# Kernel tuning notes

Hardware: AMD Instinct MI355X
Metric: run time of the kernel (lower is better)

Reference implementation:

```python
import jax, jax.numpy as jnp
import numpy as np

B, C, H, W = 16, 128, 56, 56
QK, HEADS, NWIN, TOPK, MLPR = 128, 4, 7, 4, 3
HD_Q, HD_V = QK // HEADS, C // HEADS
WH, WW = H // NWIN, W // NWIN          # 8, 8 tokens per window side
P2, W2 = NWIN * NWIN, WH * WW          # 49 regions, 64 tokens/region
SCALE = QK ** -0.5                     # BiFormer uses full qk_dim**-0.5 for both router and pixel attn


def _dwconv(x, w, b):
    # x: (B,C,H,W); w: (C,1,k,k) depthwise, odd k with SAME padding == torch padding=k//2
    y = jax.lax.conv_general_dilated(x, w, (1, 1), 'SAME',
                                     feature_group_count=x.shape[1],
                                     dimension_numbers=('NCHW', 'OIHW', 'NCHW'))
    return y + b[None, :, None, None]


def _ln(x, g, b):
    m = x.mean(-1, keepdims=True)
    v = ((x - m) ** 2).mean(-1, keepdims=True)
    return (x - m) * jax.lax.rsqrt(v + 1e-6) * g + b


def _win(t):  # (B,H,W,c) -> (B,P2,WH,WW,c)
    b, _, _, c = t.shape
    return t.reshape(b, NWIN, WH, NWIN, WW, c).transpose(0, 1, 3, 2, 4, 5).reshape(b, P2, WH, WW, c)


def _unwin(t):  # (B,P2,W2,c) -> (B,H,W,c)
    b, c = t.shape[0], t.shape[-1]
    return t.reshape(b, NWIN, NWIN, WH, WW, c).transpose(0, 1, 3, 2, 4, 5).reshape(b, H, W, c)


def setup_inputs() -> dict:
    key = jax.random.key(0)
    ks = jax.random.split(key, 8)
    p = lambda k, sh: (0.02 * jax.random.normal(k, sh)).astype(jnp.float32)
    return {
        'x': jax.random.normal(ks[0], (B, C, H, W), dtype=jnp.float32),
        'pos_w': p(ks[1], (C, 1, 3, 3)), 'pos_b': jnp.zeros((C,), jnp.float32),
        'ln1_g': jnp.ones((C,), jnp.float32), 'ln1_b': jnp.zeros((C,), jnp.float32),
        'qkv_w': p(ks[2], (C, 2 * QK + C)), 'qkv_b': jnp.zeros((2 * QK + C,), jnp.float32),
        'lepe_w': p(ks[3], (C, 1, 5, 5)), 'lepe_b': jnp.zeros((C,), jnp.float32),
        'wo_w': p(ks[4], (C, C)), 'wo_b': jnp.zeros((C,), jnp.float32),
        'ln2_g': jnp.ones((C,), jnp.float32), 'ln2_b': jnp.zeros((C,), jnp.float32),
        'mlp_w1': p(ks[5], (C, MLPR * C)), 'mlp_b1': jnp.zeros((MLPR * C,), jnp.float32),
        'mlp_w2': p(ks[6], (MLPR * C, C)), 'mlp_b2': jnp.zeros((C,), jnp.float32),
    }


def reference(x, pos_w, pos_b, ln1_g, ln1_b, qkv_w, qkv_b, lepe_w, lepe_b,
              wo_w, wo_b, ln2_g, ln2_b, mlp_w1, mlp_b1, mlp_w2, mlp_b2):
    # CPE: x = x + depthwise3x3(x)
    x = x + _dwconv(x, pos_w, pos_b)
    xh = x.transpose(0, 2, 3, 1)                        # NHWC

    # ---- BiLevelRoutingAttention(norm1(x)) ----
    y = _ln(xh, ln1_g, ln1_b)
    qkv = y @ qkv_w + qkv_b                             # (B,H,W,2*QK+C)
    q, kv = qkv[..., :QK], qkv[..., QK:]                # kv = [k | v]
    qw, kvw = _win(q), _win(kv)                         # (B,P2,WH,WW,.)

    # region-level routing: detached window means, coarse affinity, top-k regions
    q_win = jax.lax.stop_gradient(qw.mean((2, 3)))      # (B,P2,QK)
    k_win = jax.lax.stop_gradient(kvw[..., :QK].mean((2, 3)))
    logits = jnp.einsum('bpc,bqc->bpq', q_win * SCALE, k_win)
    _, idx = jax.lax.top_k(logits, TOPK)                # (B,P2,TOPK) int32

    # gather k/v tokens of the selected regions (mul_weight='none': weights unused)
    kv_pix = kvw.reshape(B, P2, W2, QK + C)
    kv_sel = jax.vmap(lambda t, i: t[i])(kv_pix, idx)   # (B,P2,TOPK,W2,QK+C)
    k_sel = kv_sel[..., :QK].reshape(B, P2, TOPK * W2, HEADS, HD_Q)
    v_sel = kv_sel[..., QK:].reshape(B, P2, TOPK * W2, HEADS, HD_V)
    q_pix = qw.reshape(B, P2, W2, HEADS, HD_Q)

    att = jnp.einsum('bpqhd,bpkhd->bphqk', q_pix * SCALE, k_sel)
    att = jax.nn.softmax(att, axis=-1)
    o = jnp.einsum('bphqk,bpkhd->bpqhd', att, v_sel).reshape(B, P2, W2, C)
    o = _unwin(o)                                       # (B,H,W,C)

    # LePE: depthwise 5x5 on v over the full image, then output projection
    v_img = kv[..., QK:].transpose(0, 3, 1, 2)
    lepe = _dwconv(v_img, lepe_w, lepe_b).transpose(0, 2, 3, 1)
    o = (o + lepe) @ wo_w + wo_b
    xh = xh + o

    # ---- MLP(norm2(x)) ----
    z = _ln(xh, ln2_g, ln2_b)
    z = jax.nn.gelu(z @ mlp_w1 + mlp_b1, approximate=False) @ mlp_w2 + mlp_b2
    xh = xh + z
    return xh.transpose(0, 3, 1, 2)                     # back to NCHW
```

## Files before the change

kernel.cpp:

```cpp
#include <hip/hip_runtime.h>
#include <math.h>

#define BATCH 16
#define CH    128
#define HGT   56
#define WID   56
#define NPIX  (BATCH*HGT*WID)
#define NQKV  384
#define NWIN  7
#define P2    49
#define TOPK  4
#define ATT_SCALE 0.088388347648318447f

typedef __attribute__((ext_vector_type(8))) short short8;
typedef __attribute__((ext_vector_type(4))) short short4v;
typedef __attribute__((ext_vector_type(4))) float float4v;

static __device__ __forceinline__ unsigned short f2bf(float f) {
  unsigned u = __float_as_uint(f);
  u += 0x7fffu + ((u >> 16) & 1u);
  return (unsigned short)(u >> 16);
}
static __device__ __forceinline__ float bf2f(unsigned short u) {
  return __uint_as_float((unsigned)u << 16);
}

__global__ __launch_bounds__(128) void k_prep(
    const float* __restrict__ qkv_w, const float* __restrict__ wo_w,
    const float* __restrict__ mlp_w1, const float* __restrict__ mlp_w2,
    unsigned short* __restrict__ Wq, unsigned short* __restrict__ Wo,
    unsigned short* __restrict__ W1, unsigned short* __restrict__ W2) {
  int bx = blockIdx.x, t = threadIdx.x;
  if (bx < 384) {
    int n = bx;
    Wq[n*128 + t] = f2bf(qkv_w[(size_t)t*384 + n]);
  } else if (bx < 512) {
    int n = bx - 384;
    Wo[n*128 + t] = f2bf(wo_w[(size_t)t*128 + n]);
  } else if (bx < 896) {
    int n = bx - 512;
    W1[n*128 + t] = f2bf(mlp_w1[(size_t)t*384 + n]);
  } else {
    int n = bx - 896;
    for (int k = t; k < 384; k += 128)
      W2[n*384 + k] = f2bf(mlp_w2[(size_t)k*128 + n]);
  }
}

__global__ __launch_bounds__(256) void k_posconv(const float* __restrict__ x,
    const float* __restrict__ pw, const float* __restrict__ pb,
    float* __restrict__ xh) {
  __shared__ float sh[10*58*32];
  int b = blockIdx.y;
  int rg = blockIdx.x >> 2, cg = blockIdx.x & 3;
  int row0 = rg*8, c0 = cg*32;
  int t = threadIdx.x;
  for (int i = t; i < 10*58*32/4; i += 256)
    ((int4*)sh)[i] = make_int4(0,0,0,0);
  __syncthreads();
  for (int i = t; i < 4480; i += 256) {
    int c = i & 31, chunk = (i >> 5) % 14, rr = i / 448;
    int grow = row0 + rr - 1;
    if ((unsigned)grow < HGT) {
      float4 v = *(const float4*)(x + ((size_t)(b*CH + c0 + c))*(HGT*WID)
                                  + grow*WID + chunk*4);
      float* d = &sh[(rr*58 + 1 + chunk*4)*32 + c];
      d[0] = v.x; d[32] = v.y; d[64] = v.z; d[96] = v.w;
    }
  }
  __syncthreads();
  int c = t & 31, pg = t >> 5;
  float w[9];
#pragma unroll
  for (int i = 0; i < 9; i++) w[i] = pw[(c0 + c)*9 + i];
  float bias = pb[c0 + c];
  const float* rowp[3];
#pragma unroll
  for (int dy = 0; dy < 3; dy++) rowp[dy] = &sh[((pg + dy)*58)*32 + c];
  float win[3][3];
#pragma unroll
  for (int j = 0; j < 2; j++)
#pragma unroll
    for (int dy = 0; dy < 3; dy++) win[j][dy] = rowp[dy][j*32];
  float* ob = &xh[(((size_t)b*HGT + row0 + pg)*WID)*CH + c0 + c];
#pragma unroll
  for (int col = 0; col < 56; col++) {
    int slot = (col + 2) % 3;
#pragma unroll
    for (int dy = 0; dy < 3; dy++) win[slot][dy] = rowp[dy][(col + 2)*32];
    float s = bias + win[(col + 1) % 3][1];
#pragma unroll
    for (int dx = 0; dx < 3; dx++) {
      int sl = (col + dx) % 3;
#pragma unroll
      for (int dy = 0; dy < 3; dy++) s += win[sl][dy] * w[dy*3 + dx];
    }
    ob[col*CH] = s;
  }
}

__global__ __launch_bounds__(256) void k_route(const float* __restrict__ xh,
    const float* __restrict__ g, const float* __restrict__ be,
    const float* __restrict__ qkv_w, const float* __restrict__ qkv_b,
    float* __restrict__ qwin, float* __restrict__ kwin) {
  __shared__ float yt[128*68];
  __shared__ float ym[128];
  int bp = blockIdx.x; int b = bp / P2, p = bp % P2;
  int wy = p / NWIN, wx = p % NWIN;
  int t = threadIdx.x;
  int pl = t >> 2, qu = t & 3;
  {
    int hg = wy*8 + (pl >> 3), wg = wx*8 + (pl & 7);
    const float4* src = (const float4*)(xh + (((size_t)b*HGT + hg)*WID + wg)*CH + qu*32);
    float v[32]; float s = 0.f, ss = 0.f;
#pragma unroll
    for (int i = 0; i < 8; i++) {
      float4 f = src[i];
      v[4*i] = f.x; v[4*i+1] = f.y; v[4*i+2] = f.z; v[4*i+3] = f.w;
      s += f.x + f.y + f.z + f.w;
      ss += f.x*f.x + f.y*f.y + f.z*f.z + f.w*f.w;
    }
    s += __shfl_xor(s, 1); ss += __shfl_xor(ss, 1);
    s += __shfl_xor(s, 2); ss += __shfl_xor(ss, 2);
    float m  = s * (1.f/128.f);
    float var = ss * (1.f/128.f) - m*m;
    float rs = rsqrtf(var + 1e-6f);
#pragma unroll
    for (int i = 0; i < 32; i++) {
      int ch = qu*32 + i;
      yt[ch*68 + pl] = (v[i] - m) * rs * g[ch] + be[ch];
    }
  }
  __syncthreads();
  if (t < 128) {
    const float4* col = (const float4*)&yt[t*68];
    float4 a = make_float4(0.f,0.f,0.f,0.f);
#pragma unroll
    for (int i = 0; i < 16; i++) {
      float4 f = col[i];
      a.x += f.x; a.y += f.y; a.z += f.z; a.w += f.w;
    }
    ym[t] = (a.x + a.y + a.z + a.w) * (1.f/64.f);
  }
  __syncthreads();
  {
    int n = t;
    float s = qkv_b[n];
#pragma unroll 4
    for (int c = 0; c < 128; c++) s += ym[c] * qkv_w[(size_t)c*NQKV + n];
    if (n < 128) qwin[(size_t)bp*128 + n] = s;
    else         kwin[(size_t)bp*128 + n - 128] = s;
  }
}

__global__ __launch_bounds__(256) void k_topk(const float* __restrict__ qwin,
    const float* __restrict__ kwin, int* __restrict__ idx) {
  __shared__ float logits[64];
  int bp = blockIdx.x; int b = bp / P2;
  int t = threadIdx.x;
  int key = t >> 2, qu = t & 3;
  float s = 0.f;
  if (key < P2) {
    const float4* qp = (const float4*)(qwin + (size_t)bp*128 + qu*32);
    const float4* kp = (const float4*)(kwin + ((size_t)b*P2 + key)*128 + qu*32);
#pragma unroll
    for (int i = 0; i < 8; i++) {
      float4 qv = qp[i], kv = kp[i];
      s += qv.x*kv.x + qv.y*kv.y + qv.z*kv.z + qv.w*kv.w;
    }
  }
  s += __shfl_xor(s, 1);
  s += __shfl_xor(s, 2);
  if (qu == 0 && key < P2) logits[key] = s;
  __syncthreads();
  if (t == 0) {
    unsigned long long used = 0ULL;
    for (int tt = 0; tt < TOPK; tt++) {
      float best = -1e30f; int bi = 0;
      for (int q = 0; q < P2; q++) {
        bool ok = !((used >> q) & 1ULL);
        float lv = logits[q];
        if (ok && lv > best) { best = lv; bi = q; }
      }
      used |= 1ULL << bi;
      idx[(size_t)bp*TOPK + tt] = bi;
    }
  }
}

__global__ __launch_bounds__(256, 2) void k_qkv_gemm(
    const float* __restrict__ in, const float* __restrict__ g,
    const float* __restrict__ be, const unsigned short* __restrict__ Wt,
    const float* __restrict__ bias,
    unsigned short* __restrict__ qW, unsigned short* __restrict__ kW,
    unsigned short* __restrict__ vT) {
  __shared__ __align__(16) unsigned short aL[128*136];
  __shared__ __align__(16) unsigned short bL[128*136];
  int base = blockIdx.x * 128;
  int t = threadIdx.x;
  {
    int r = t >> 1, half = t & 1;
    const float4* src = (const float4*)(in + (size_t)(base + r)*CH + half*64);
    float v[64];
    float s = 0.f, ss = 0.f;
#pragma unroll
    for (int i = 0; i < 16; i++) {
      float4 f = src[i];
      v[4*i] = f.x; v[4*i+1] = f.y; v[4*i+2] = f.z; v[4*i+3] = f.w;
      s += f.x + f.y + f.z + f.w;
      ss += f.x*f.x + f.y*f.y + f.z*f.z + f.w*f.w;
    }
    s += __shfl_xor(s, 1); ss += __shfl_xor(ss, 1);
    float m  = s * (1.f/128.f);
    float var = ss * (1.f/128.f) - m*m;
    float rs = rsqrtf(var + 1e-6f);
    union { unsigned short us[8]; int4 v4; } pk;
#pragma unroll
    for (int c8 = 0; c8 < 8; c8++) {
#pragma unroll
      for (int j = 0; j < 8; j++) {
        int ch = half*64 + c8*8 + j;
        pk.us[j] = f2bf((v[c8*8 + j] - m) * rs * g[ch] + be[ch]);
      }
      *(int4*)&aL[r*136 + half*64 + c8*8] = pk.v4;
    }
  }
  int wid = t >> 6, lane = t & 63;
  int ln = lane & 15, q = lane >> 4;
  int wr = (wid >> 1)*64, wc = (wid & 1)*64;
  for (int chunk = 0; chunk < 3; chunk++) {
    if (chunk) __syncthreads();
    for (int i = t; i < 2048; i += 256) {
      int row = i >> 4, seg = i & 15;
      *(int4*)&bL[row*136 + seg*8] =
          *(const int4*)(Wt + (size_t)(chunk*128 + row)*128 + seg*8);
    }
    __syncthreads();
    float4v acc[4][4];
#pragma unroll
    for (int a = 0; a < 4; a++)
#pragma unroll
      for (int b2 = 0; b2 < 4; b2++)
        acc[a][b2] = (float4v){0.f, 0.f, 0.f, 0.f};
#pragma unroll
    for (int kk = 0; kk < 4; kk++) {
      int ko = kk*32 + q*8;
      short8 af[4], bf[4];
#pragma unroll
      for (int mf = 0; mf < 4; mf++)
        af[mf] = *(const short8*)&aL[(wr + mf*16 + ln)*136 + ko];
#pragma unroll
      for (int nf = 0; nf < 4; nf++)
        bf[nf] = *(const short8*)&bL[(wc + nf*16 + ln)*136 + ko];
#pragma unroll
      for (int mf = 0; mf < 4; mf++)
#pragma unroll
        for (int nf = 0; nf < 4; nf++)
          acc[mf][nf] = __builtin_amdgcn_mfma_f32_16x16x32_bf16(
              af[mf], bf[nf], acc[mf][nf], 0, 0, 0);
    }
    if (chunk < 2) {
      unsigned short* dst = chunk ? kW : qW;
      float sc = chunk ? 1.f : ATT_SCALE;
#pragma unroll
      for (int mf = 0; mf < 4; mf++) {
#pragma unroll
        for (int j = 0; j < 4; j++) {
          int pg = base + wr + mf*16 + q*4 + j;
          int b  = pg / 3136, sp = pg - b*3136;
          int hh = sp / 56, ww = sp - hh*56;
          int p  = (hh >> 3)*NWIN + (ww >> 3);
          int ploc = (hh & 7)*8 + (ww & 7);
          size_t rb = ((size_t)(b*P2 + p)*64 + ploc)*128;
#pragma unroll
          for (int nf = 0; nf < 4; nf++) {
            int col = wc + nf*16 + ln;
            dst[rb + col] = f2bf((acc[mf][nf][j] + bias[chunk*128 + col])*sc);
          }
        }
      }
    } else {
      __syncthreads();
#pragma unroll
      for (int mf = 0; mf < 4; mf++)
#pragma unroll
        for (int nf = 0; nf < 4; nf++) {
          int row = wr + mf*16 + q*4;
          int col = wc + nf*16 + ln;
          float b4 = bias[256 + col];
          short4v pk;
#pragma unroll
          for (int j = 0; j < 4; j++) pk[j] = (short)f2bf(acc[mf][nf][j] + b4);
          *(short4v*)&aL[col*136 + row] = pk;
        }
      __syncthreads();
      int c = t >> 1, half = t & 1;
#pragma unroll
      for (int g8 = 0; g8 < 8; g8++) {
        int pg0 = base + half*64 + g8*8;
        int b = pg0 / 3136, sp = pg0 - b*3136;
        *(int4*)(vT + ((size_t)(b*CH + c))*3136 + sp) =
            *(int4*)&aL[c*136 + half*64 + g8*8];
      }
    }
  }
}

#define PLS 72
__global__ __launch_bounds__(256) void k_attn_mfma(
    const unsigned short* __restrict__ qW, const unsigned short* __restrict__ kW,
    const unsigned short* __restrict__ vT, const int* __restrict__ idx,
    unsigned short* __restrict__ o) {
  __shared__ unsigned short pL[4][64*PLS];
  int bx = blockIdx.x;
  int b = bx & 15, p = bx >> 4;
  int bp = b*P2 + p;
  int wy = p / NWIN, wx = p % NWIN;
  int h = threadIdx.x >> 6, lane = threadIdx.x & 63;
  int ln = lane & 15, q = lane >> 4;

  short8 aq[4];
#pragma unroll
  for (int mf = 0; mf < 4; mf++)
    aq[mf] = *(const short8*)&qW[((size_t)bp*64 + mf*16 + ln)*128 + h*32 + q*8];

  int4 widx = *(const int4*)&idx[(size_t)bp*TOPK];
  int wins[4] = {widx.x, widx.y, widx.z, widx.w};

  float l_run[4][4];
  float4v facc[4][2];
#pragma unroll
  for (int mf = 0; mf < 4; mf++) {
#pragma unroll
    for (int j = 0; j < 4; j++) l_run[mf][j] = 0.f;
    facc[mf][0] = (float4v){0.f,0.f,0.f,0.f};
    facc[mf][1] = (float4v){0.f,0.f,0.f,0.f};
  }

  unsigned short* myP = &pL[h][0];
  int swr = ((ln >> 2) & 3) * 16;

  for (int r = 0; r < TOPK; r++) {
    int win = wins[r];
    int sy = win / NWIN, sx = win % NWIN;
    short8 bk[4];
#pragma unroll
    for (int nf = 0; nf < 4; nf++)
      bk[nf] = *(const short8*)&kW[(((size_t)b*P2 + win)*64 + nf*16 + ln)*128 + h*32 + q*8];
    float4v sacc[4][4];
#pragma unroll
    for (int mf = 0; mf < 4; mf++)
#pragma unroll
      for (int nf = 0; nf < 4; nf++)
        sacc[mf][nf] = (float4v){0.f,0.f,0.f,0.f};
#pragma unroll
    for (int mf = 0; mf < 4; mf++)
#pragma unroll
      for (int nf = 0; nf < 4; nf++)
        sacc[mf][nf] = __builtin_amdgcn_mfma_f32_16x16x32_bf16(
            aq[mf], bk[nf], sacc[mf][nf], 0, 0, 0);
#pragma unroll
    for (int mf = 0; mf < 4; mf++) {
#pragma unroll
      for (int j = 0; j < 4; j++) {
        float e0 = __expf(sacc[mf][0][j]);
        float e1 = __expf(sacc[mf][1][j]);
        float e2 = __expf(sacc[mf][2][j]);
        float e3 = __expf(sacc[mf][3][j]);
        l_run[mf][j] += (e0 + e1) + (e2 + e3);
        int rowoff = (mf*16 + q*4 + j)*PLS;
        int sww = q*16;
        myP[rowoff + (( 0 + ln) ^ sww)] = f2bf(e0);
        myP[rowoff + ((16 + ln) ^ sww)] = f2bf(e1);
        myP[rowoff + ((32 + ln) ^ sww)] = f2bf(e2);
        myP[rowoff + ((48 + ln) ^ sww)] = f2bf(e3);
      }
    }
#pragma unroll
    for (int kk = 0; kk < 2; kk++) {
      short8 ap[4];
#pragma unroll
      for (int mf = 0; mf < 4; mf++)
        ap[mf] = *(const short8*)&myP[(mf*16 + ln)*PLS + ((kk*32 + q*8) ^ swr)];
      short8 bv[2];
#pragma unroll
      for (int nf2 = 0; nf2 < 2; nf2++) {
        int d = h*32 + nf2*16 + ln;
        int K0 = kk*32 + q*8;
        const unsigned short* vp = vT + ((size_t)b*CH + d)*(HGT*WID)
            + (sy*8 + (K0 >> 3))*WID + sx*8;
        bv[nf2] = *(const short8*)vp;
      }
#pragma unroll
      for (int mf = 0; mf < 4; mf++)
#pragma unroll
        for (int nf2 = 0; nf2 < 2; nf2++)
          facc[mf][nf2] = __builtin_amdgcn_mfma_f32_16x16x32_bf16(
              ap[mf], bv[nf2], facc[mf][nf2], 0, 0, 0);
    }
  }
#pragma unroll
  for (int mf = 0; mf < 4; mf++)
#pragma unroll
    for (int j = 0; j < 4; j++) {
      float l = l_run[mf][j];
      l += __shfl_xor(l, 1);
      l += __shfl_xor(l, 2);
      l += __shfl_xor(l, 4);
      l += __shfl_xor(l, 8);
      float inv = 1.f / l;
      int prow = mf*16 + q*4 + j;
      size_t pg = ((size_t)b*HGT + wy*8 + (prow>>3))*WID + wx*8 + (prow&7);
      o[pg*CH + h*32 + ln]      = f2bf(facc[mf][0][j] * inv);
      o[pg*CH + h*32 + 16 + ln] = f2bf(facc[mf][1][j] * inv);
    }
}

__global__ __launch_bounds__(256) void k_lepe(const unsigned short* __restrict__ vT,
    const float* __restrict__ lw, const float* __restrict__ lb,
    unsigned short* __restrict__ o) {
  __shared__ unsigned short sh[12*60*32];
  int b = blockIdx.y;
  int rg = blockIdx.x >> 2, cg = blockIdx.x & 3;
  int row0 = rg*8, c0 = cg*32;
  int t = threadIdx.x;
  for (int i = t; i < 12*60*32/8; i += 256)
    ((int4*)sh)[i] = make_int4(0,0,0,0);
  __syncthreads();
  for (int i = t; i < 2688; i += 256) {
    int chunk = i % 7, rr = (i/7) % 12, c = i / 84;
    int grow = row0 + rr - 2;
    if ((unsigned)grow < HGT) {
      int4 v = *(const int4*)(vT + ((size_t)(b*CH + c0 + c))*(HGT*WID) + grow*WID + chunk*8);
      union { int4 v4; unsigned short us[8]; } u; u.v4 = v;
#pragma unroll
      for (int j = 0; j < 8; j++)
        sh[(rr*60 + 2 + chunk*8 + j)*32 + c] = u.us[j];
    }
  }
  __syncthreads();
  int c = t & 31, pg = t >> 5;
  float w[25];
#pragma unroll
  for (int i = 0; i < 25; i++) w[i] = lw[(c0 + c)*25 + i];
  float bias = lb[c0 + c];
  const unsigned short* rowp[5];
#pragma unroll
  for (int dy = 0; dy < 5; dy++) rowp[dy] = &sh[((pg + dy)*60)*32 + c];
  float win[5][5];
#pragma unroll
  for (int j = 0; j < 4; j++)
#pragma unroll
    for (int dy = 0; dy < 5; dy++) win[j][dy] = bf2f(rowp[dy][j*32]);
  unsigned short* ob = &o[(((size_t)b*HGT + row0 + pg)*WID)*CH + c0 + c];
#pragma unroll
  for (int col = 0; col < 56; col++) {
    int slot = (col + 4) % 5;
#pragma unroll
    for (int dy = 0; dy < 5; dy++) win[slot][dy] = bf2f(rowp[dy][(col + 4)*32]);
    float s = bias;
#pragma unroll
    for (int dx = 0; dx < 5; dx++) {
      int sl = (col + dx) % 5;
#pragma unroll
      for (int dy = 0; dy < 5; dy++) s += win[sl][dy] * w[dy*5 + dx];
    }
    unsigned short* p = &ob[col*CH];
    *p = f2bf(bf2f(*p) + s);
  }
}

__global__ __launch_bounds__(256, 2) void k_wo_mfma(
    const unsigned short* __restrict__ in, const unsigned short* __restrict__ Wt,
    const float* __restrict__ bias, float* __restrict__ xh) {
  __shared__ __align__(16) unsigned short aL[128*136];
  __shared__ __align__(16) unsigned short bL[128*136];
  size_t base = (size_t)blockIdx.x * 128;
  int t = threadIdx.x;
  {
    int r = t >> 1, half = t & 1;
    const int4* src = (const int4*)(in + (base + r)*CH + half*64);
#pragma unroll
    for (int i = 0; i < 8; i++)
      *(int4*)&aL[r*136 + half*64 + i*8] = src[i];
  }
  for (int i = t; i < 2048; i += 256) {
    int row = i >> 4, seg = i & 15;
    *(int4*)&bL[row*136 + seg*8] = *(const int4*)(Wt + (size_t)row*128 + seg*8);
  }
  __syncthreads();
  int wid = t >> 6, lane = t & 63;
  int ln = lane & 15, q = lane >> 4;
  int wr = (wid >> 1)*64, wc = (wid & 1)*64;
  float4v acc[4][4];
#pragma unroll
  for (int a = 0; a < 4; a++)
#pragma unroll
    for (int b = 0; b < 4; b++)
      acc[a][b] = (float4v){0.f, 0.f, 0.f, 0.f};
#pragma unroll
  for (int kk = 0; kk < 4; kk++) {
    int ko = kk*32 + q*8;
    short8 af[4], bf[4];
#pragma unroll
    for (int mf = 0; mf < 4; mf++)
      af[mf] = *(const short8*)&aL[(wr + mf*16 + ln)*136 + ko];
#pragma unroll
    for (int nf = 0; nf < 4; nf++)
      bf[nf] = *(const short8*)&bL[(wc + nf*16 + ln)*136 + ko];
#pragma unroll
    for (int mf = 0; mf < 4; mf++)
#pragma unroll
      for (int nf = 0; nf < 4; nf++)
        acc[mf][nf] = __builtin_amdgcn_mfma_f32_16x16x32_bf16(
            af[mf], bf[nf], acc[mf][nf], 0, 0, 0);
  }
#pragma unroll
  for (int mf = 0; mf < 4; mf++)
#pragma unroll
    for (int nf = 0; nf < 4; nf++) {
      int row = wr + mf*16 + q*4;
      int col = wc + nf*16 + ln;
      float b4 = bias[col];
#pragma unroll
      for (int j = 0; j < 4; j++) {
        float* p = &xh[(base + row + j)*CH + col];
        *p += acc[mf][nf][j] + b4;
      }
    }
}

__global__ __launch_bounds__(256, 2) void k_mlp1_gemm(
    const float* __restrict__ in, const float* __restrict__ g,
    const float* __restrict__ be, const unsigned short* __restrict__ Wt,
    const float* __restrict__ bias, unsigned short* __restrict__ hidb) {
  __shared__ __align__(16) unsigned short aL[128*136];
  __shared__ __align__(16) unsigned short bL[128*136];
  size_t base = (size_t)blockIdx.x * 128;
  int t = threadIdx.x;
  {
    int r = t >> 1, half = t & 1;
    const float4* src = (const float4*)(in + (base + r)*CH + half*64);
    float v[64];
    float s = 0.f, ss = 0.f;
#pragma unroll
    for (int i = 0; i < 16; i++) {
      float4 f = src[i];
      v[4*i] = f.x; v[4*i+1] = f.y; v[4*i+2] = f.z; v[4*i+3] = f.w;
      s += f.x + f.y + f.z + f.w;
      ss += f.x*f.x + f.y*f.y + f.z*f.z + f.w*f.w;
    }
    s += __shfl_xor(s, 1); ss += __shfl_xor(ss, 1);
    float m  = s * (1.f/128.f);
    float var = ss * (1.f/128.f) - m*m;
    float rs = rsqrtf(var + 1e-6f);
    union { unsigned short us[8]; int4 v4; } pk;
#pragma unroll
    for (int c8 = 0; c8 < 8; c8++) {
#pragma unroll
      for (int j = 0; j < 8; j++) {
        int ch = half*64 + c8*8 + j;
        pk.us[j] = f2bf((v[c8*8 + j] - m) * rs * g[ch] + be[ch]);
      }
      *(int4*)&aL[r*136 + half*64 + c8*8] = pk.v4;
    }
  }
  int wid = t >> 6, lane = t & 63;
  int ln = lane & 15, q = lane >> 4;
  int wr = (wid >> 1)*64, wc = (wid & 1)*64;
  for (int chunk = 0; chunk < 3; chunk++) {
    if (chunk) __syncthreads();
    for (int i = t; i < 2048; i += 256) {
      int row = i >> 4, seg = i & 15;
      *(int4*)&bL[row*136 + seg*8] =
          *(const int4*)(Wt + (size_t)(chunk*128 + row)*128 + seg*8);
    }
    __syncthreads();
    float4v acc[4][4];
#pragma unroll
    for (int a = 0; a < 4; a++)
#pragma unroll
      for (int b = 0; b < 4; b++)
        acc[a][b] = (float4v){0.f, 0.f, 0.f, 0.f};
#pragma unroll
    for (int kk = 0; kk < 4; kk++) {
      int ko = kk*32 + q*8;
      short8 af[4], bf[4];
#pragma unroll
      for (int mf = 0; mf < 4; mf++)
        af[mf] = *(const short8*)&aL[(wr + mf*16 + ln)*136 + ko];
#pragma unroll
      for (int nf = 0; nf < 4; nf++)
        bf[nf] = *(const short8*)&bL[(wc + nf*16 + ln)*136 + ko];
#pragma unroll
      for (int mf = 0; mf < 4; mf++)
#pragma unroll
        for (int nf = 0; nf < 4; nf++)
          acc[mf][nf] = __builtin_amdgcn_mfma_f32_16x16x32_bf16(
              af[mf], bf[nf], acc[mf][nf], 0, 0, 0);
    }
#pragma unroll
    for (int mf = 0; mf < 4; mf++)
#pragma unroll
      for (int nf = 0; nf < 4; nf++) {
        int row = wr + mf*16 + q*4;
        int col = wc + nf*16 + ln + chunk*128;
        float b4 = bias[col];
#pragma unroll
        for (int j = 0; j < 4; j++) {
          float vv = acc[mf][nf][j] + b4;
          vv = 0.5f * vv * (1.f + erff(vv * 0.70710678118654752f));
          hidb[(base + row + j)*NQKV + col] = f2bf(vv);
        }
      }
  }
}

__global__ __launch_bounds__(256, 2) void k_mlp2_mfma(
    const unsigned short* __restrict__ hidb, const unsigned short* __restrict__ Wt,
    const float* __restrict__ bias, const float* __restrict__ xh,
    float* __restrict__ out) {
  __shared__ __align__(16) unsigned short aL[128*136];
  __shared__ __align__(16) unsigned short bL[128*136];
  size_t base = (size_t)blockIdx.x * 128;
  int t = threadIdx.x;
  int wid = t >> 6, lane = t & 63;
  int ln = lane & 15, q = lane >> 4;
  int wr = (wid >> 1)*64, wc = (wid & 1)*64;
  float4v acc[4][4];
#pragma unroll
  for (int a = 0; a < 4; a++)
#pragma unroll
    for (int b = 0; b < 4; b++)
      acc[a][b] = (float4v){0.f, 0.f, 0.f, 0.f};
  for (int kc = 0; kc < 3; kc++) {
    if (kc) __syncthreads();
    {
      int r = t >> 1, half = t & 1;
      const int4* src = (const int4*)(hidb + (base + r)*NQKV + kc*128 + half*64);
#pragma unroll
      for (int i = 0; i < 8; i++)
        *(int4*)&aL[r*136 + half*64 + i*8] = src[i];
    }
    for (int i = t; i < 2048; i += 256) {
      int row = i >> 4, seg = i & 15;
      *(int4*)&bL[row*136 + seg*8] =
          *(const int4*)(Wt + (size_t)row*NQKV + kc*128 + seg*8);
    }
    __syncthreads();
#pragma unroll
    for (int kk = 0; kk < 4; kk++) {
      int ko = kk*32 + q*8;
      short8 af[4], bf[4];
#pragma unroll
      for (int mf = 0; mf < 4; mf++)
        af[mf] = *(const short8*)&aL[(wr + mf*16 + ln)*136 + ko];
#pragma unroll
      for (int nf = 0; nf < 4; nf++)
        bf[nf] = *(const short8*)&bL[(wc + nf*16 + ln)*136 + ko];
#pragma unroll
      for (int mf = 0; mf < 4; mf++)
#pragma unroll
        for (int nf = 0; nf < 4; nf++)
          acc[mf][nf] = __builtin_amdgcn_mfma_f32_16x16x32_bf16(
              af[mf], bf[nf], acc[mf][nf], 0, 0, 0);
    }
  }
#pragma unroll
  for (int mf = 0; mf < 4; mf++)
#pragma unroll
    for (int nf = 0; nf < 4; nf++) {
      int row = wr + mf*16 + q*4;
      int col = wc + nf*16 + ln;
      float b4 = bias[col];
#pragma unroll
      for (int j = 0; j < 4; j++) {
        size_t pixel = base + row + j;
        int b = (int)(pixel / (HGT*WID));
        int sp = (int)(pixel % (HGT*WID));
        out[((size_t)b*CH + col)*(HGT*WID) + sp] =
            acc[mf][nf][j] + b4 + xh[pixel*CH + col];
      }
    }
}

extern "C" void kernel_launch(void* const* d_in, const int* in_sizes, int n_in,
                              void* d_out, int out_size, void* d_ws, size_t ws_size,
                              hipStream_t stream) {
  const float* x      = (const float*)d_in[0];
  const float* pos_w  = (const float*)d_in[1];
  const float* pos_b  = (const float*)d_in[2];
  const float* ln1_g  = (const float*)d_in[3];
  const float* ln1_b  = (const float*)d_in[4];
  const float* qkv_w  = (const float*)d_in[5];
  const float* qkv_b  = (const float*)d_in[6];
  const float* lepe_w = (const float*)d_in[7];
  const float* lepe_b = (const float*)d_in[8];
  const float* wo_w   = (const float*)d_in[9];
  const float* wo_b   = (const float*)d_in[10];
  const float* ln2_g  = (const float*)d_in[11];
  const float* ln2_b  = (const float*)d_in[12];
  const float* mlp_w1 = (const float*)d_in[13];
  const float* mlp_b1 = (const float*)d_in[14];
  const float* mlp_w2 = (const float*)d_in[15];
  const float* mlp_b2 = (const float*)d_in[16];

  float* ws   = (float*)d_ws;
  float* xh   = ws;
  float* o_slot = xh + (size_t)NPIX*CH;
  unsigned short* obf = (unsigned short*)o_slot;
  float* qwin = o_slot + (size_t)NPIX*CH;
  float* kwin = qwin + (size_t)BATCH*P2*128;
  int*   idx  = (int*)(kwin + (size_t)BATCH*P2*128);
  unsigned short* Wq = (unsigned short*)(idx + BATCH*P2*TOPK);
  unsigned short* Wo = Wq + 384*128;
  unsigned short* W1 = Wo + 128*128;
  unsigned short* W2 = W1 + 384*128;
  unsigned short* vT = W2 + 128*384;
  unsigned short* qW = vT + (size_t)NPIX*CH;
  unsigned short* kW = qW + (size_t)NPIX*CH;
  unsigned short* hidb = kW + (size_t)NPIX*CH;

  k_prep<<<1024, 128, 0, stream>>>(qkv_w, wo_w, mlp_w1, mlp_w2, Wq, Wo, W1, W2);
  k_posconv<<<dim3(28, BATCH), 256, 0, stream>>>(x, pos_w, pos_b, xh);
  k_route<<<BATCH*P2, 256, 0, stream>>>(xh, ln1_g, ln1_b, qkv_w, qkv_b, qwin, kwin);
  k_topk<<<BATCH*P2, 256, 0, stream>>>(qwin, kwin, idx);
  k_qkv_gemm<<<NPIX/128, 256, 0, stream>>>(xh, ln1_g, ln1_b, Wq, qkv_b, qW, kW, vT);
  k_attn_mfma<<<BATCH*P2, 256, 0, stream>>>(qW, kW, vT, idx, obf);
  k_lepe<<<dim3(28, BATCH), 256, 0, stream>>>(vT, lepe_w, lepe_b, obf);
  k_wo_mfma<<<NPIX/128, 256, 0, stream>>>(obf, Wo, wo_b, xh);
  k_mlp1_gemm<<<NPIX/128, 256, 0, stream>>>(xh, ln2_g, ln2_b, W1, mlp_b1, hidb);
  k_mlp2_mfma<<<NPIX/128, 256, 0, stream>>>(hidb, W2, mlp_b2, xh, (float*)d_out);
}
```

Baseline: 327.6 us.

## Fuse MLP fc1 and fc2 into one kernel keeping hidden chunks in LDS

Merges the two MLP GEMM kernels into one. Each 128-column chunk of the GELU hidden activation is written to shared memory and consumed right away by the second GEMM, so the bf16 hidden tensor no longer makes a round trip through global memory and one launch is saved. The weight tiles are no longer staged in LDS; the MFMA B fragments are read directly from global memory (through cache), which may cost more load latency per fragment. The fused kernel also holds two sets of accumulators, raising register pressure.

Result: faster. 319.1 us, median of 2 (-2.6%).

```diff
diff --git a/kernel.cpp b/kernel.cpp
--- a/kernel.cpp
+++ b/kernel.cpp
@@ -530,12 +530,13 @@
     }
 }
 
-__global__ __launch_bounds__(256, 2) void k_mlp1_gemm(
+__global__ __launch_bounds__(256, 2) void k_mlp(
     const float* __restrict__ in, const float* __restrict__ g,
-    const float* __restrict__ be, const unsigned short* __restrict__ Wt,
-    const float* __restrict__ bias, unsigned short* __restrict__ hidb) {
+    const float* __restrict__ be, const unsigned short* __restrict__ W1t,
+    const float* __restrict__ b1, const unsigned short* __restrict__ W2t,
+    const float* __restrict__ b2, float* __restrict__ out) {
   __shared__ __align__(16) unsigned short aL[128*136];
-  __shared__ __align__(16) unsigned short bL[128*136];
+  __shared__ __align__(16) unsigned short cL[128*136];
   size_t base = (size_t)blockIdx.x * 128;
   int t = threadIdx.x;
   {
@@ -565,23 +566,23 @@
       *(int4*)&aL[r*136 + half*64 + c8*8] = pk.v4;
     }
   }
+  __syncthreads();
   int wid = t >> 6, lane = t & 63;
   int ln = lane & 15, q = lane >> 4;
   int wr = (wid >> 1)*64, wc = (wid & 1)*64;
+  float4v acc2[4][4];
+#pragma unroll
+  for (int a = 0; a < 4; a++)
+#pragma unroll
+    for (int b = 0; b < 4; b++)
+      acc2[a][b] = (float4v){0.f, 0.f, 0.f, 0.f};
   for (int chunk = 0; chunk < 3; chunk++) {
-    if (chunk) __syncthreads();
-    for (int i = t; i < 2048; i += 256) {
-      int row = i >> 4, seg = i & 15;
-      *(int4*)&bL[row*136 + seg*8] =
-          *(const int4*)(Wt + (size_t)(chunk*128 + row)*128 + seg*8);
-    }
-    __syncthreads();
-    float4v acc[4][4];
+    float4v acc1[4][4];
 #pragma unroll
     for (int a = 0; a < 4; a++)
 #pragma unroll
       for (int b = 0; b < 4; b++)
-        acc[a][b] = (float4v){0.f, 0.f, 0.f, 0.f};
+        acc1[a][b] = (float4v){0.f, 0.f, 0.f, 0.f};
 #pragma unroll
     for (int kk = 0; kk < 4; kk++) {
       int ko = kk*32 + q*8;
@@ -591,62 +592,29 @@
         af[mf] = *(const short8*)&aL[(wr + mf*16 + ln)*136 + ko];
 #pragma unroll
       for (int nf = 0; nf < 4; nf++)
-        bf[nf] = *(const short8*)&bL[(wc + nf*16 + ln)*136 + ko];
+        bf[nf] = *(const short8*)&W1t[(size_t)(chunk*128 + wc + nf*16 + ln)*128 + ko];
 #pragma unroll
       for (int mf = 0; mf < 4; mf++)
 #pragma unroll
         for (int nf = 0; nf < 4; nf++)
-          acc[mf][nf] = __builtin_amdgcn_mfma_f32_16x16x32_bf16(
-              af[mf], bf[nf], acc[mf][nf], 0, 0, 0);
-    }
+          acc1[mf][nf] = __builtin_amdgcn_mfma_f32_16x16x32_bf16(
+              af[mf], bf[nf], acc1[mf][nf], 0, 0, 0);
+    }
+    __syncthreads();
 #pragma unroll
     for (int mf = 0; mf < 4; mf++)
 #pragma unroll
       for (int nf = 0; nf < 4; nf++) {
         int row = wr + mf*16 + q*4;
-        int col = wc + nf*16 + ln + chunk*128;
-        float b4 = bias[col];
+        int col = wc + nf*16 + ln;
+        float b4 = b1[chunk*128 + col];
 #pragma unroll
         for (int j = 0; j < 4; j++) {
-          float vv = acc[mf][nf][j] + b4;
+          float vv = acc1[mf][nf][j] + b4;
           vv = 0.5f * vv * (1.f + erff(vv * 0.70710678118654752f));
-          hidb[(base + row + j)*NQKV + col] = f2bf(vv);
+          cL[(row + j)*136 + col] = f2bf(vv);
         }
       }
-  }
-}
-
-__global__ __launch_bounds__(256, 2) void k_mlp2_mfma(
-    const unsigned short* __restrict__ hidb, const unsigned short* __restrict__ Wt,
-    const float* __restrict__ bias, const float* __restrict__ xh,
-    float* __restrict__ out) {
-  __shared__ __align__(16) unsigned short aL[128*136];
-  __shared__ __align__(16) unsigned short bL[128*136];
-  size_t base = (size_t)blockIdx.x * 128;
-  int t = threadIdx.x;
-  int wid = t >> 6, lane = t & 63;
-  int ln = lane & 15, q = lane >> 4;
-  int wr = (wid >> 1)*64, wc = (wid & 1)*64;
-  float4v acc[4][4];
-#pragma unroll
-  for (int a = 0; a < 4; a++)
-#pragma unroll
-    for (int b = 0; b < 4; b++)
-      acc[a][b] = (float4v){0.f, 0.f, 0.f, 0.f};
-  for (int kc = 0; kc < 3; kc++) {
-    if (kc) __syncthreads();
-    {
-      int r = t >> 1, half = t & 1;
-      const int4* src = (const int4*)(hidb + (base + r)*NQKV + kc*128 + half*64);
-#pragma unroll
-      for (int i = 0; i < 8; i++)
-        *(int4*)&aL[r*136 + half*64 + i*8] = src[i];
-    }
-    for (int i = t; i < 2048; i += 256) {
-      int row = i >> 4, seg = i & 15;
-      *(int4*)&bL[row*136 + seg*8] =
-          *(const int4*)(Wt + (size_t)row*NQKV + kc*128 + seg*8);
-    }
     __syncthreads();
 #pragma unroll
     for (int kk = 0; kk < 4; kk++) {
@@ -654,16 +622,16 @@
       short8 af[4], bf[4];
 #pragma unroll
       for (int mf = 0; mf < 4; mf++)
-        af[mf] = *(const short8*)&aL[(wr + mf*16 + ln)*136 + ko];
+        af[mf] = *(const short8*)&cL[(wr + mf*16 + ln)*136 + ko];
 #pragma unroll
       for (int nf = 0; nf < 4; nf++)
-        bf[nf] = *(const short8*)&bL[(wc + nf*16 + ln)*136 + ko];
+        bf[nf] = *(const short8*)&W2t[(size_t)(wc + nf*16 + ln)*NQKV + chunk*128 + ko];
 #pragma unroll
       for (int mf = 0; mf < 4; mf++)
 #pragma unroll
         for (int nf = 0; nf < 4; nf++)
-          acc[mf][nf] = __builtin_amdgcn_mfma_f32_16x16x32_bf16(
-              af[mf], bf[nf], acc[mf][nf], 0, 0, 0);
+          acc2[mf][nf] = __builtin_amdgcn_mfma_f32_16x16x32_bf16(
+              af[mf], bf[nf], acc2[mf][nf], 0, 0, 0);
     }
   }
 #pragma unroll
@@ -672,14 +640,14 @@
     for (int nf = 0; nf < 4; nf++) {
       int row = wr + mf*16 + q*4;
       int col = wc + nf*16 + ln;
-      float b4 = bias[col];
+      float b4 = b2[col];
 #pragma unroll
       for (int j = 0; j < 4; j++) {
         size_t pixel = base + row + j;
         int b = (int)(pixel / (HGT*WID));
         int sp = (int)(pixel % (HGT*WID));
         out[((size_t)b*CH + col)*(HGT*WID) + sp] =
-            acc[mf][nf][j] + b4 + xh[pixel*CH + col];
+            acc2[mf][nf][j] + b4 + in[pixel*CH + col];
       }
     }
 }
@@ -719,7 +687,6 @@
   unsigned short* vT = W2 + 128*384;
   unsigned short* qW = vT + (size_t)NPIX*CH;
   unsigned short* kW = qW + (size_t)NPIX*CH;
-  unsigned short* hidb = kW + (size_t)NPIX*CH;
 
   k_prep<<<1024, 128, 0, stream>>>(qkv_w, wo_w, mlp_w1, mlp_w2, Wq, Wo, W1, W2);
   k_posconv<<<dim3(28, BATCH), 256, 0, stream>>>(x, pos_w, pos_b, xh);
@@ -729,6 +696,6 @@
   k_attn_mfma<<<BATCH*P2, 256, 0, stream>>>(qW, kW, vT, idx, obf);
   k_lepe<<<dim3(28, BATCH), 256, 0, stream>>>(vT, lepe_w, lepe_b, obf);
   k_wo_mfma<<<NPIX/128, 256, 0, stream>>>(obf, Wo, wo_b, xh);
-  k_mlp1_gemm<<<NPIX/128, 256, 0, stream>>>(xh, ln2_g, ln2_b, W1, mlp_b1, hidb);
-  k_mlp2_mfma<<<NPIX/128, 256, 0, stream>>>(hidb, W2, mlp_b2, xh, (float*)d_out);
-}
+  k_mlp<<<NPIX/128, 256, 0, stream>>>(xh, ln2_g, ln2_b, W1, mlp_b1, W2, mlp_b2,
+                                      (float*)d_out);
+}
```
